# Performance work log

Hardware: AMD Instinct MI355X
Metric: run time of the kernel (lower is better)

## Reference

```python
import jax, jax.numpy as jnp
import numpy as np
from jax import lax

DN = ('NCHW', 'OIHW', 'NCHW')


def _conv(x, w, b):
    # SAME-padded 3x3 conv; bias broadcast over spatial dims
    y = lax.conv_general_dilated(x, w, (1, 1), 'SAME', dimension_numbers=DN)
    return y + b[None, :, None, None]


def setup_inputs() -> dict:
    key = jax.random.key(0)
    ks = jax.random.split(key, 6)
    B, Cin, Ch, H, W, K = 8, 16, 32, 256, 256, 3
    fan = (Cin + Ch) * K * K
    scale = 1.0 / np.sqrt(fan)
    return {
        'x': jax.random.normal(ks[0], (B, Cin, H, W), jnp.float32),
        'prev': jax.random.normal(ks[1], (B, Ch, H, W), jnp.float32),
        'mask': jax.random.randint(ks[2], (B, 1, H, W), 0, 2, jnp.int32),
        'w_reset': jax.random.normal(ks[3], (Ch, Cin + Ch, K, K), jnp.float32) * scale,
        'b_reset': jnp.zeros((Ch,), jnp.float32),
        'w_update': jax.random.normal(ks[4], (Ch, Cin + Ch, K, K), jnp.float32) * scale,
        'b_update': jnp.zeros((Ch,), jnp.float32),
        'w_out': jax.random.normal(ks[5], (Ch, Cin + Ch, K, K), jnp.float32) * scale,
        'b_out': jnp.zeros((Ch,), jnp.float32),
    }


def reference(x, prev, mask, w_reset, b_reset, w_update, b_update, w_out, b_out):
    # Dense emulation of submanifold sparse ConvGRU: features exist only at
    # active sites (mask==1); convs gather zeros from inactive sites (matching
    # SCN's rule-based gather) and outputs/biases are masked to active sites.
    m = mask.astype(x.dtype)  # [B,1,H,W] active-site indicator
    x = x * m
    prev = prev * m
    stacked = jnp.concatenate([x, prev], axis=1)  # [B, Cin+Ch, H, W]
    update = jax.nn.sigmoid(_conv(stacked, w_update, b_update)) * m
    reset = jax.nn.sigmoid(_conv(stacked, w_reset, b_reset)) * m
    stacked_r = jnp.concatenate([x, prev * reset], axis=1)
    out_inputs = jnp.tanh(_conv(stacked_r, w_out, b_out)) * m
    # new_state = prev*(1-update) + out_inputs*update (zero off active set)
    new_state = prev * (1.0 - update) + out_inputs * update
    return new_state
```

## Files before the change

kernel.cpp:

```cpp
#include <hip/hip_runtime.h>
#include <hip/hip_bf16.h>
#include <math.h>

#define HH 256
#define WW 256
#define CIN 16
#define CHID 32
#define CST 48
#define HWPIX (HH * WW)

#define TSX 32
#define TSY 16
#define HX 36
#define HY 20
#define NPX (HX * HY)
#define SP 56
#define NKS 14
#define RNX 34
#define RNY 18
#define RPOS (RNX * RNY)
#define EPS 524

typedef unsigned short u16;
typedef unsigned int u32;
typedef __attribute__((ext_vector_type(8))) short short8;
typedef __attribute__((ext_vector_type(8))) __bf16 bf16x8;
typedef __attribute__((ext_vector_type(4))) float f32x4;
typedef __attribute__((ext_vector_type(2))) float f32x2;
typedef __attribute__((ext_vector_type(4))) unsigned int u32x4;

__device__ __forceinline__ float b2f(u16 h) {
    union { unsigned u; float f; } v; v.u = ((unsigned)h) << 16; return v.f;
}
__device__ __forceinline__ u16 f2b(float f) {
    union { float f; unsigned u; } v; v.f = f;
    unsigned r = v.u + 0x7fffu + ((v.u >> 16) & 1u);
    return (u16)(r >> 16);
}
__device__ __forceinline__ u32 pk2(float a, float bq) {
    u32 r;
    asm("v_cvt_pk_bf16_f32 %0, %1, %2" : "=v"(r) : "v"(a), "v"(bq));
    return r;
}
__device__ __forceinline__ int imin(int a, int b) { return a < b ? a : b; }

__global__ void packb_kernel(const float* __restrict__ wR, const float* __restrict__ wU,
                             const float* __restrict__ wO,
                             const float* __restrict__ bR, const float* __restrict__ bU,
                             const float* __restrict__ bO, u16* __restrict__ pB) {
    int i = blockIdx.x * 256 + threadIdx.x;
    const int TOT = 3 * NKS * 2 * 64 * 8;
    if (i >= TOT) return;
    int conv = i / (NKS * 2 * 64 * 8);
    int r = i - conv * (NKS * 2 * 64 * 8);
    int ks = r / (2 * 64 * 8); r -= ks * (2 * 64 * 8);
    int nf = r / (64 * 8);     r -= nf * (64 * 8);
    int lane = r >> 3, j = r & 7;
    int k = ks * 32 + (lane >> 4) * 8 + j;
    int n = nf * 16 + (lane & 15);
    float scale = (conv == 2) ? 2.885390082f : -1.442695041f;
    float val = 0.f;
    if (k < 432) {
        int tap = k / 48, ci = k - tap * 48;
        const float* w = (conv == 0) ? wR : (conv == 1) ? wU : wO;
        val = w[(n * CST + ci) * 9 + tap] * scale;
    } else if (k == 432) {
        const float* bb = (conv == 0) ? bR : (conv == 1) ? bU : bO;
        val = bb[n] * scale;
    }
    pB[i] = f2b(val);
}

__global__ __launch_bounds__(512, 4) void convgru_mfma(
    const float* __restrict__ x, const float* __restrict__ prev,
    const int* __restrict__ mask, const u16* __restrict__ pB,
    float* __restrict__ out)
{
    __shared__ __align__(16) u16 s1[NPX * SP];
    __shared__ unsigned char smask8[NPX];
    float* sEp = (float*)s1;

    const int flat = (blockIdx.z * gridDim.y + blockIdx.y) * gridDim.x + blockIdx.x;
    const int wid  = ((flat & 7) << 7) | (flat >> 3);
    const int b    = wid >> 7;
    const int y0   = ((wid >> 3) & 15) * TSY;
    const int x0   = (wid & 7) * TSX;

    const int tid = threadIdx.x;
    const int w    = tid >> 6;
    const int lane = tid & 63;
    const int run  = lane >> 4;
    const int lo   = lane & 15;

    #pragma unroll
    for (int rp = 0; rp < 2; rp++) {
        int p = rp * 512 + tid;
        bool act = p < NPX;
        int pc = act ? p : (NPX - 1);
        int yy = (pc * 911) >> 15;
        int xx = pc - yy * HX;
        int gy = y0 + yy - 2, gx = x0 + xx - 2;
        bool in = (unsigned)gy < HH && (unsigned)gx < WW;
        int gyc = in ? gy : 0, gxc = in ? gx : 0;
        int mi = in ? mask[(b * HH + gyc) * WW + gxc] : 0;
        float mv = (float)mi;
        if (act) {
            smask8[pc] = (unsigned char)mi;
            const float* xb = x    + (size_t)b * CIN  * HWPIX + gyc * WW + gxc;
            const float* pb = prev + (size_t)b * CHID * HWPIX + gyc * WW + gxc;
            u32* dst = (u32*)&s1[pc * SP];
            #pragma unroll
            for (int g = 0; g < 6; g++) {
                const float* src = (g < 2) ? (xb + g * 8 * HWPIX)
                                           : (pb + (g * 8 - 16) * HWPIX);
                u32x4 w4;
                #pragma unroll
                for (int h = 0; h < 4; h++) {
                    float v0 = src[(2 * h)     * HWPIX] * mv;
                    float v1 = src[(2 * h + 1) * HWPIX] * mv;
                    w4[h] = pk2(v0, v1);
                }
                *(u32x4*)(dst + g * 4) = w4;
            }
            *(u32x4*)(dst + 24) = (u32x4){0x3f80u, 0u, 0u, 0u};
        }
    }
    __syncthreads();

    int koff[NKS];
    #pragma unroll
    for (int ks = 0; ks < NKS; ks++) {
        int klin = ks * 4 + run;
        int tap = imin((klin * 43) >> 8, 8);
        int ci  = imin((klin - tap * 6) * 8, 40);
        int ky = (tap * 11) >> 5, kx = tap - ky * 3;
        int off = (((ky * HX + kx) * SP) + ci) * 2;
        if (klin == 54) off = ((HX + 1) * SP + 48) * 2;
        koff[ks] = off;
    }

    const char* s1c = (const char*)s1;
    const short8* pB8 = (const short8*)pB;
    const f32x4 z4 = {0.f, 0.f, 0.f, 0.f};
    const int baseU = (((2 * w) + 1) * HX + 1 + lo) * SP * 2;
    const int fOffB[4] = {0, 16 * SP * 2, HX * SP * 2, (HX + 16) * SP * 2};

    f32x4 accU[4][2];
    #pragma unroll
    for (int f = 0; f < 4; f++) { accU[f][0] = z4; accU[f][1] = z4; }
    {
        short8 bp[2][2];
        bp[0][0] = pB8[(1 * NKS + 0) * 128 + lane];
        bp[0][1] = pB8[(1 * NKS + 0) * 128 + 64 + lane];
        bp[1][0] = pB8[(1 * NKS + 1) * 128 + lane];
        bp[1][1] = pB8[(1 * NKS + 1) * 128 + 64 + lane];
        #pragma unroll
        for (int ks = 0; ks < NKS; ks++) {
            short8 b0 = bp[ks & 1][0], b1 = bp[ks & 1][1];
            if (ks + 2 < NKS) {
                bp[ks & 1][0] = pB8[(1 * NKS + ks + 2) * 128 + lane];
                bp[ks & 1][1] = pB8[(1 * NKS + ks + 2) * 128 + 64 + lane];
            }
            const char* ap = s1c + baseU + koff[ks];
            __builtin_amdgcn_s_setprio(1);
            #pragma unroll
            for (int f = 0; f < 4; f++) {
                short8 av = *(const short8*)(ap + fOffB[f]);
                bf16x8 a = __builtin_bit_cast(bf16x8, av);
                accU[f][0] = __builtin_amdgcn_mfma_f32_16x16x32_bf16(a, __builtin_bit_cast(bf16x8, b0), accU[f][0], 0, 0, 0);
                accU[f][1] = __builtin_amdgcn_mfma_f32_16x16x32_bf16(a, __builtin_bit_cast(bf16x8, b1), accU[f][1], 0, 0, 0);
            }
            __builtin_amdgcn_s_setprio(0);
        }
    }

    f32x4 accR[5][2];
    #pragma unroll
    for (int f = 0; f < 5; f++) { accR[f][0] = z4; accR[f][1] = z4; }

    int pbase[5];
    #pragma unroll
    for (int f = 0; f < 5; f++) {
        int frag = w + f * 8;
        int idx = imin(frag * 16 + lo, RPOS - 1);
        int ry = (idx * 241) >> 13;
        int rx = idx - ry * RNX;
        pbase[f] = (ry * HX + rx) * SP * 2;
    }
    {
        short8 bp[2][2];
        bp[0][0] = pB8[(0 * NKS + 0) * 128 + lane];
        bp[0][1] = pB8[(0 * NKS + 0) * 128 + 64 + lane];
        bp[1][0] = pB8[(0 * NKS + 1) * 128 + lane];
        bp[1][1] = pB8[(0 * NKS + 1) * 128 + 64 + lane];
        #pragma unroll
        for (int ks = 0; ks < NKS; ks++) {
            short8 b0 = bp[ks & 1][0], b1 = bp[ks & 1][1];
            if (ks + 2 < NKS) {
                bp[ks & 1][0] = pB8[(0 * NKS + ks + 2) * 128 + lane];
                bp[ks & 1][1] = pB8[(0 * NKS + ks + 2) * 128 + 64 + lane];
            }
            __builtin_amdgcn_s_setprio(1);
            #pragma unroll
            for (int f = 0; f < 5; f++) {
                if (f == 4 && w == 7) continue;
                short8 av = *(const short8*)(s1c + pbase[f] + koff[ks]);
                bf16x8 a = __builtin_bit_cast(bf16x8, av);
                accR[f][0] = __builtin_amdgcn_mfma_f32_16x16x32_bf16(a, __builtin_bit_cast(bf16x8, b0), accR[f][0], 0, 0, 0);
                accR[f][1] = __builtin_amdgcn_mfma_f32_16x16x32_bf16(a, __builtin_bit_cast(bf16x8, b1), accR[f][1], 0, 0, 0);
            }
            __builtin_amdgcn_s_setprio(0);
        }
    }

    unsigned pms[4][4];
    #pragma unroll
    for (int f = 0; f < 4; f++) {
        int row = 2 * w + (f >> 1);
        int xh  = (f & 1) * 16;
        #pragma unroll
        for (int reg = 0; reg < 4; reg++) {
            int px = xh + run * 4 + reg;
            int base = ((row + 2) * HX + px + 2) * SP + CIN + lo;
            unsigned a0 = s1[base];
            unsigned a1 = s1[base + 16];
            pms[f][reg] = a0 | (a1 << 16);
        }
    }
    __syncthreads();

    {
        #pragma unroll
        for (int f = 0; f < 5; f++) {
            if (f == 4 && w == 7) continue;
            int frag = w + f * 8;
            #pragma unroll
            for (int reg = 0; reg < 4; reg++) {
                int idx = frag * 16 + run * 4 + reg;
                bool valid = idx < RPOS;
                int idc = imin(idx, RPOS - 1);
                int ry = (idc * 241) >> 13, rx = idc - ry * RNX;
                int base = ((ry + 1) * HX + rx + 1) * SP + CIN + lo;
                float sg0 = __builtin_amdgcn_rcpf(1.f + exp2f(accR[f][0][reg]));
                float sg1 = __builtin_amdgcn_rcpf(1.f + exp2f(accR[f][1][reg]));
                float pm0 = b2f(s1[base]);
                float pm1 = b2f(s1[base + 16]);
                u32 pkres = pk2(pm0 * sg0, pm1 * sg1);
                if (valid) {
                    s1[base]      = (u16)pkres;
                    s1[base + 16] = (u16)(pkres >> 16);
                }
            }
        }
    }
    __syncthreads();

    f32x4 accO[4][2];
    #pragma unroll
    for (int f = 0; f < 4; f++) { accO[f][0] = z4; accO[f][1] = z4; }
    {
        short8 bp[2][2];
        bp[0][0] = pB8[(2 * NKS + 0) * 128 + lane];
        bp[0][1] = pB8[(2 * NKS + 0) * 128 + 64 + lane];
        bp[1][0] = pB8[(2 * NKS + 1) * 128 + lane];
        bp[1][1] = pB8[(2 * NKS + 1) * 128 + 64 + lane];
        #pragma unroll
        for (int ks = 0; ks < NKS; ks++) {
            short8 b0 = bp[ks & 1][0], b1 = bp[ks & 1][1];
            if (ks + 2 < NKS) {
                bp[ks & 1][0] = pB8[(2 * NKS + ks + 2) * 128 + lane];
                bp[ks & 1][1] = pB8[(2 * NKS + ks + 2) * 128 + 64 + lane];
            }
            const char* ap = s1c + baseU + koff[ks];
            __builtin_amdgcn_s_setprio(1);
            #pragma unroll
            for (int f = 0; f < 4; f++) {
                short8 av = *(const short8*)(ap + fOffB[f]);
                bf16x8 a = __builtin_bit_cast(bf16x8, av);
                accO[f][0] = __builtin_amdgcn_mfma_f32_16x16x32_bf16(a, __builtin_bit_cast(bf16x8, b0), accO[f][0], 0, 0, 0);
                accO[f][1] = __builtin_amdgcn_mfma_f32_16x16x32_bf16(a, __builtin_bit_cast(bf16x8, b1), accO[f][1], 0, 0, 0);
            }
            __builtin_amdgcn_s_setprio(0);
        }
    }
    __syncthreads();

    {
        #pragma unroll
        for (int f = 0; f < 4; f++) {
            int row = 2 * w + (f >> 1);
            int xh  = (f & 1) * 16;
            #pragma unroll
            for (int rp = 0; rp < 2; rp++) {
                int px0 = xh + run * 4 + rp * 2;
                float mm = (float)smask8[(row + 2) * HX + px0 + 2];
                #pragma unroll
                for (int nf = 0; nf < 2; nf++) {
                    int c = nf * 16 + lo;
                    f32x2 ov;
                    #pragma unroll
                    for (int q = 0; q < 2; q++) {
                        int reg = rp * 2 + q;
                        float mq = (float)smask8[(row + 2) * HX + (xh + run * 4 + reg) + 2];
                        float su = __builtin_amdgcn_rcpf(1.f + exp2f(accU[f][nf][reg]));
                        float th = fmaf(-2.f, __builtin_amdgcn_rcpf(1.f + exp2f(accO[f][nf][reg])), 1.f);
                        float pm = b2f((u16)((pms[f][reg] >> (nf * 16)) & 0xffffu));
                        ov[q] = fmaf(su, fmaf(mq, th, -pm), pm);
                    }
                    *(f32x2*)&sEp[c * EPS + row * TSX + px0] = ov;
                }
            }
        }
    }
    __syncthreads();

    #pragma unroll
    for (int r = 0; r < 8; r++) {
        int i = r * 512 + tid;
        int c = i >> 7;
        int q = (i & 127) * 4;
        f32x4 v = *(const f32x4*)&sEp[c * EPS + q];
        int row = q >> 5, col = q & 31;
        *(f32x4*)&out[((size_t)(b * CHID + c) * HH + y0 + row) * WW + x0 + col] = v;
    }
}

extern "C" void kernel_launch(void* const* d_in, const int* in_sizes, int n_in,
                              void* d_out, int out_size, void* d_ws, size_t ws_size,
                              hipStream_t stream) {
    const float* x       = (const float*)d_in[0];
    const float* prev    = (const float*)d_in[1];
    const int*   mask    = (const int*)d_in[2];
    const float* w_reset = (const float*)d_in[3];
    const float* b_reset = (const float*)d_in[4];
    const float* w_upd   = (const float*)d_in[5];
    const float* b_upd   = (const float*)d_in[6];
    const float* w_out   = (const float*)d_in[7];
    const float* b_out   = (const float*)d_in[8];
    float* out = (float*)d_out;

    u16* pB = (u16*)d_ws;
    const int TOT = 3 * NKS * 2 * 64 * 8;
    packb_kernel<<<(TOT + 255) / 256, 256, 0, stream>>>(w_reset, w_upd, w_out,
                                                        b_reset, b_upd, b_out, pB);

    dim3 grid(WW / TSX, HH / TSY, 8);
    convgru_mfma<<<grid, 512, 0, stream>>>(x, prev, mask, pB, out);
}
```

Before: 81.50 us.

## Overlap prev-channel staging loads with update-gate MFMA k-steps

Reorders the K dimension so the x channels and bias come first and the prev channels follow in two chunks of 16. The initial LDS fill now writes only x; prev channels are loaded from global memory into registers, and the first update-conv k-steps run while those loads are in flight. The data is then packed into LDS with extra barriers between chunks. This hides global-load latency behind MFMA work, at the cost of more registers (32 floats held live) and two extra block-wide syncs.

```diff
diff --git a/kernel.cpp b/kernel.cpp
--- a/kernel.cpp
+++ b/kernel.cpp
@@ -21,6 +21,7 @@
 #define RPOS (RNX * RNY)
 #define EPS 524
 
+
 typedef unsigned short u16;
 typedef unsigned int u32;
 typedef __attribute__((ext_vector_type(8))) short short8;
@@ -55,16 +56,20 @@
     int r = i - conv * (NKS * 2 * 64 * 8);
     int ks = r / (2 * 64 * 8); r -= ks * (2 * 64 * 8);
     int nf = r / (64 * 8);     r -= nf * (64 * 8);
-    int lane = r >> 3, j = r & 7;
-    int k = ks * 32 + (lane >> 4) * 8 + j;
+    int lane = r >> 3, j8 = r & 7;
+    int klin = ks * 4 + (lane >> 4);
     int n = nf * 16 + (lane & 15);
     float scale = (conv == 2) ? 2.885390082f : -1.442695041f;
     float val = 0.f;
-    if (k < 432) {
-        int tap = k / 48, ci = k - tap * 48;
+    if (klin < 18 || klin >= 20) {
+        int cib, tap;
+        if (klin >= 38)      { int j = klin - 38; int h = j >= 9; cib = 4 + h; tap = j - h * 9; }
+        else if (klin >= 20) { int j = klin - 20; int h = j >= 9; cib = 2 + h; tap = j - h * 9; }
+        else                 { int h = klin >= 9; cib = h; tap = klin - h * 9; }
+        int ci = cib * 8 + j8;
         const float* w = (conv == 0) ? wR : (conv == 1) ? wU : wO;
         val = w[(n * CST + ci) * 9 + tap] * scale;
-    } else if (k == 432) {
+    } else if (klin == 18 && j8 == 0) {
         const float* bb = (conv == 0) ? bR : (conv == 1) ? bU : bO;
         val = bb[n] * scale;
     }
@@ -92,10 +97,14 @@
     const int run  = lane >> 4;
     const int lo   = lane & 15;
 
+    bool act1 = (512 + tid) < NPX;
+    float mv_[2];
+    const float* pb_[2];
+
     #pragma unroll
     for (int rp = 0; rp < 2; rp++) {
         int p = rp * 512 + tid;
-        bool act = p < NPX;
+        bool act = (rp == 0) | act1;
         int pc = act ? p : (NPX - 1);
         int yy = (pc * 911) >> 15;
         int xx = pc - yy * HX;
@@ -104,15 +113,15 @@
         int gyc = in ? gy : 0, gxc = in ? gx : 0;
         int mi = in ? mask[(b * HH + gyc) * WW + gxc] : 0;
         float mv = (float)mi;
+        mv_[rp] = mv;
+        const float* xb = x + (size_t)b * CIN * HWPIX + gyc * WW + gxc;
+        pb_[rp] = prev + (size_t)b * CHID * HWPIX + gyc * WW + gxc;
         if (act) {
             smask8[pc] = (unsigned char)mi;
-            const float* xb = x    + (size_t)b * CIN  * HWPIX + gyc * WW + gxc;
-            const float* pb = prev + (size_t)b * CHID * HWPIX + gyc * WW + gxc;
             u32* dst = (u32*)&s1[pc * SP];
             #pragma unroll
-            for (int g = 0; g < 6; g++) {
-                const float* src = (g < 2) ? (xb + g * 8 * HWPIX)
-                                           : (pb + (g * 8 - 16) * HWPIX);
+            for (int g = 0; g < 2; g++) {
+                const float* src = xb + g * 8 * HWPIX;
                 u32x4 w4;
                 #pragma unroll
                 for (int h = 0; h < 4; h++) {
@@ -131,11 +140,17 @@
     #pragma unroll
     for (int ks = 0; ks < NKS; ks++) {
         int klin = ks * 4 + run;
-        int tap = imin((klin * 43) >> 8, 8);
-        int ci  = imin((klin - tap * 6) * 8, 40);
-        int ky = (tap * 11) >> 5, kx = tap - ky * 3;
-        int off = (((ky * HX + kx) * SP) + ci) * 2;
-        if (klin == 54) off = ((HX + 1) * SP + 48) * 2;
+        int off;
+        if (klin >= 18 && klin < 20) {
+            off = ((HX + 1) * SP + 48) * 2;
+        } else {
+            int cib, tap;
+            if (klin >= 38)      { int j = klin - 38; int h = j >= 9; cib = 4 + h; tap = j - h * 9; }
+            else if (klin >= 20) { int j = klin - 20; int h = j >= 9; cib = 2 + h; tap = j - h * 9; }
+            else                 { int h = klin >= 9; cib = h; tap = klin - h * 9; }
+            int ky = (tap * 11) >> 5, kx = tap - ky * 3;
+            off = (((ky * HX + kx) * SP) + cib * 8) * 2;
+        }
         koff[ks] = off;
     }
 
@@ -154,8 +169,8 @@
         bp[0][1] = pB8[(1 * NKS + 0) * 128 + 64 + lane];
         bp[1][0] = pB8[(1 * NKS + 1) * 128 + lane];
         bp[1][1] = pB8[(1 * NKS + 1) * 128 + 64 + lane];
-        #pragma unroll
-        for (int ks = 0; ks < NKS; ks++) {
+
+        auto U_KS = [&](int ks) {
             short8 b0 = bp[ks & 1][0], b1 = bp[ks & 1][1];
             if (ks + 2 < NKS) {
                 bp[ks & 1][0] = pB8[(1 * NKS + ks + 2) * 128 + lane];
@@ -171,7 +186,66 @@
                 accU[f][1] = __builtin_amdgcn_mfma_f32_16x16x32_bf16(a, __builtin_bit_cast(bf16x8, b1), accU[f][1], 0, 0, 0);
             }
             __builtin_amdgcn_s_setprio(0);
-        }
+        };
+
+        {
+            float pv[2][16];
+            #pragma unroll
+            for (int rp = 0; rp < 2; rp++) {
+                const float* pbp = pb_[rp];
+                #pragma unroll
+                for (int h = 0; h < 16; h++) pv[rp][h] = pbp[h * HWPIX];
+            }
+            #pragma unroll
+            for (int ks = 0; ks < 5; ks++) U_KS(ks);
+            #pragma unroll
+            for (int rp = 0; rp < 2; rp++) {
+                if ((rp == 0) | act1) {
+                    u32* dst = (u32*)&s1[(rp * 512 + tid) * SP];
+                    float mv = mv_[rp];
+                    u32x4 w4a, w4b;
+                    #pragma unroll
+                    for (int h = 0; h < 4; h++) {
+                        w4a[h] = pk2(pv[rp][2 * h] * mv, pv[rp][2 * h + 1] * mv);
+                        w4b[h] = pk2(pv[rp][8 + 2 * h] * mv, pv[rp][8 + 2 * h + 1] * mv);
+                    }
+                    *(u32x4*)(dst + 8)  = w4a;
+                    *(u32x4*)(dst + 12) = w4b;
+                }
+            }
+            __syncthreads();
+        }
+
+        {
+            float pv[2][16];
+            #pragma unroll
+            for (int rp = 0; rp < 2; rp++) {
+                const float* pbp = pb_[rp] + 16 * HWPIX;
+                #pragma unroll
+                for (int h = 0; h < 16; h++) pv[rp][h] = pbp[h * HWPIX];
+            }
+            #pragma unroll
+            for (int ks = 5; ks < 9; ks++) U_KS(ks);
+            #pragma unroll
+            for (int rp = 0; rp < 2; rp++) {
+                if ((rp == 0) | act1) {
+                    u32* dst = (u32*)&s1[(rp * 512 + tid) * SP];
+                    float mv = mv_[rp];
+                    u32x4 w4a, w4b;
+                    #pragma unroll
+                    for (int h = 0; h < 4; h++) {
+                        w4a[h] = pk2(pv[rp][2 * h] * mv, pv[rp][2 * h + 1] * mv);
+                        w4b[h] = pk2(pv[rp][8 + 2 * h] * mv, pv[rp][8 + 2 * h + 1] * mv);
+                    }
+                    *(u32x4*)(dst + 16) = w4a;
+                    *(u32x4*)(dst + 20) = w4b;
+                }
+            }
+            __syncthreads();
+        }
+
+        #pragma unroll
+        for (int ks = 9; ks < NKS; ks++) U_KS(ks);
     }
 
     f32x4 accR[5][2];
@@ -291,16 +365,15 @@
             int row = 2 * w + (f >> 1);
             int xh  = (f & 1) * 16;
             #pragma unroll
-            for (int rp = 0; rp < 2; rp++) {
-                int px0 = xh + run * 4 + rp * 2;
-                float mm = (float)smask8[(row + 2) * HX + px0 + 2];
+            for (int rp2 = 0; rp2 < 2; rp2++) {
+                int px0 = xh + run * 4 + rp2 * 2;
                 #pragma unroll
                 for (int nf = 0; nf < 2; nf++) {
                     int c = nf * 16 + lo;
                     f32x2 ov;
                     #pragma unroll
                     for (int q = 0; q < 2; q++) {
-                        int reg = rp * 2 + q;
+                        int reg = rp2 * 2 + q;
                         float mq = (float)smask8[(row + 2) * HX + (xh + run * 4 + reg) + 2];
                         float su = __builtin_amdgcn_rcpf(1.f + exp2f(accU[f][nf][reg]));
                         float th = fmaf(-2.f, __builtin_amdgcn_rcpf(1.f + exp2f(accO[f][nf][reg])), 1.f);
```

Measured after the change: 90.53 us. 11.1% more time.
